# Optimization experiments

Hardware: AMD Instinct MI355X
Metric: run time of the kernel (lower is better)

Reference implementation:

```python
import jax, jax.numpy as jnp
import numpy as np

A, NA, D_OBS, B = 16, 8, 64, 128  # agents, actions, obs dim, graphs
DZ = D_OBS + NA  # obs_z_input_dim = 72


def _mlp(x, W1, b1, W2, b2):
    # Linear -> leaky_relu(0.01) -> Linear, torch Linear convention (y = x @ W.T + b)
    return jax.nn.leaky_relu(x @ W1.T + b1) @ W2.T + b2


def setup_inputs() -> dict:
    key = jax.random.key(0)
    ks = iter(jax.random.split(key, 40))
    p = {}
    p["obs"] = jax.random.normal(next(ks), (B * A, D_OBS), jnp.float32)
    p["policies"] = jax.random.uniform(next(ks), (B * A, NA), jnp.float32)
    p["actions"] = jax.random.uniform(next(ks), (B * A, NA), jnp.float32)

    def mk(name, inp, out):
        p[name + "_w"] = jax.random.normal(next(ks), (out, inp), jnp.float32) / np.sqrt(inp).astype(np.float32)
        p[name + "_b"] = jax.random.normal(next(ks), (out,), jnp.float32) * 0.01

    mk("kw1", D_OBS, 64); mk("kw2", 64, 64)   # key_weight layers
    mk("qw1", D_OBS, 64); mk("qw2", 64, 64)   # query_weight layers
    mk("ko1", DZ, 64);    mk("ko2", 64, 64)   # key_obsz layers
    mk("qo1", DZ, 64);    mk("qo2", 64, 64)   # query_obsz layers
    mk("av1", DZ, 64);    mk("av2", 64, 64)   # attention_value_obsz layers
    mk("fv1", 128, 64);   mk("fv2", 64, 8)    # final_value layers
    return p


def reference(obs, policies, actions,
              kw1_w, kw1_b, kw2_w, kw2_b, qw1_w, qw1_b, qw2_w, qw2_b,
              ko1_w, ko1_b, ko2_w, ko2_b, qo1_w, qo1_b, qo2_w, qo2_b,
              av1_w, av1_b, av2_w, av2_b, fv1_w, fv1_b, fv2_w, fv2_b):
    d_k_w = jnp.sqrt(jnp.float32(kw2_w.shape[0]))
    d_k_o = jnp.sqrt(jnp.float32(ko2_w.shape[0]))
    Bn = obs.shape[0] // A
    obs_b = obs.reshape(Bn, A, -1)                      # [B,A,Dobs]
    pi = policies.reshape(Bn, A, NA)
    act = actions.reshape(Bn, A, NA)

    # --- DGL update_all on the fully-connected (with self-loop) per-batch graph ---
    key_z = _mlp(obs_b, kw1_w, kw1_b, kw2_w, kw2_b)     # [B,A,dk]
    query_z = _mlp(obs_b, qw1_w, qw1_b, qw2_w, qw2_b)
    score = jnp.einsum('bjd,bid->bij', key_z, query_z)  # src key j -> dst query i
    w = jax.nn.sigmoid(score / d_k_w)[..., None]        # [B,A,A,1], mailbox gate
    z = w * act[:, None] + (1.0 - w) * pi[:, None]      # [B,A(i),A(j),NA]
    weight_z = w.reshape(Bn * A, A, 1)

    # obs_z[b,i,j] = cat(obs[b,j], z[b,i,j])
    obs_rep = jnp.broadcast_to(obs_b[:, None], (Bn, A, A, obs_b.shape[-1]))
    obs_z = jnp.concatenate([obs_rep, z], axis=-1)      # [B,A,A,DZ]

    diag = jnp.arange(A)
    src = obs_z[:, diag, diag]                          # source_obs_z_: [B,A,DZ] (j==i entry)

    key_o = _mlp(src, ko1_w, ko1_b, ko2_w, ko2_b)       # broadcast over j
    query_o = _mlp(obs_z, qo1_w, qo1_b, qo2_w, qo2_b)   # [B,A,A,dk]
    score_o = jnp.einsum('bid,bijd->bij', key_o, query_o)
    weights_o = jax.nn.softmax(jnp.exp(jnp.clip(score_o / d_k_o, -5.0, 5.0)), axis=-1)  # [B,A,A]

    # obs_z_pi[b,i,j,k] = op[b,j] if k==j else obs_z[b,i,k], op = cat(obs, pi)
    op = jnp.concatenate([obs_b, pi], axis=-1)          # [B,A,DZ]
    m = jnp.eye(A, dtype=obs.dtype)[None, None, :, :, None]          # (j,k) mask
    obs_z_pi = obs_z[:, :, None] * (1.0 - m) + op[:, None, None] * m  # [B,A,A,A,DZ]

    attn_src = _mlp(src, av1_w, av1_b, av2_w, av2_b)                  # [B,A,O]
    attn_other = _mlp(obs_z_pi, av1_w, av1_b, av2_w, av2_b)           # [B,A,A,A,O]

    w_exp = weights_o[:, None, :, :, None]              # [b,i,j,k,1] = weights_o[b,j,k]
    mixed = jnp.mean(attn_other * w_exp, axis=-2)       # mean over k -> [B,A,A,O]
    src_rep = jnp.broadcast_to(attn_src[:, None], mixed.shape)
    node_features = jnp.concatenate([src_rep, mixed], axis=-1)        # [B,A,A,2O]
    value = _mlp(node_features, fv1_w, fv1_b, fv2_w, fv2_b)           # [B,A,A,8]

    weights_obsz = jnp.broadcast_to(w_exp, (Bn, A, A, A, 1))
    return value, weight_z, weights_obsz
```

## Files before the change

### kernel.cpp

```cpp
#include <hip/hip_runtime.h>

#define A_ 16
#define NA_ 8
#define DOBS_ 64

typedef _Float16 f16;
typedef f16 h2 __attribute__((ext_vector_type(2)));
typedef f16 v8h __attribute__((ext_vector_type(8)));
typedef float v4f __attribute__((ext_vector_type(4)));

__device__ __forceinline__ float fdot2f(h2 a, h2 b, float c) {
  return __builtin_amdgcn_fdot2(a, b, c, false);
}
__device__ __forceinline__ float lrelu(float x) { return x > 0.f ? x : 0.01f * x; }

struct P {
  const float *obs, *pol, *act;
  const float *kw1w, *kw1b, *kw2w, *kw2b, *qw1w, *qw1b, *qw2w, *qw2b;
  const float *ko1w, *ko1b, *ko2w, *ko2b, *qo1w, *qo1b, *qo2w, *qo2b;
  const float *av1w, *av1b, *av2w, *av2b, *fv1w, *fv1b, *fv2w, *fv2b;
  float *out0, *out1, *out2;
};

struct alignas(16) SM {
  f16 obsh[16 * 72];
  float pi[128];
  float act[128];
  float wsig[256];
  float wo[256];
  float c0[16];
  f16 eh[256];
  union {
    struct {
      f16 obsl[16 * 72];
      f16 Wp1[64 * 72], Wp2[64 * 72];
      f16 Wxh[64 * 72], Wxl[64 * 72];
      f16 X1h[16 * 72], X1l[16 * 72];
      f16 X2h[16 * 72], X2l[16 * 72];
      float S2[16 * 68];
      float S3G[16 * 68];
      float wz[512];
    } f;
    struct {
      f16 AOsrcD[16 * 72];
      f16 APT[64 * 24];
      f16 AextH[16 * 40];
      f16 fv2pw[512];
      f16 slice[8][1536];
      union { struct { f16 av1H[64 * 96]; f16 av2H[64 * 72]; } av; f16 fv1H[64 * 136]; } W;
      float av1b[64], av2b[64], fv1b[64], fv2b[8];
    } bk;
  } u;
};

__device__ __forceinline__ v4f gemm_plain(const f16* Xh, const f16* W, float bv, int nt, int lane) {
  const int m = lane & 15, q = lane >> 4;
  v4f acc = {bv, bv, bv, bv};
  const v8h a0 = *(const v8h*)(Xh + m * 72 + q * 8);
  const v8h a1 = *(const v8h*)(Xh + m * 72 + 32 + q * 8);
  const f16* wr = W + (nt * 16 + m) * 72 + q * 8;
  acc = __builtin_amdgcn_mfma_f32_16x16x32_f16(a0, *(const v8h*)wr, acc, 0, 0, 0);
  acc = __builtin_amdgcn_mfma_f32_16x16x32_f16(a1, *(const v8h*)(wr + 32), acc, 0, 0, 0);
  return acc;
}

__device__ __forceinline__ v4f gemm_tile(const f16* Xh, const f16* Xl,
                                         const f16* Wh, const f16* Wl,
                                         float bv, int nt, int lane) {
  const int m = lane & 15, q = lane >> 4;
  v4f acc = {bv, bv, bv, bv};
  const v8h ah0 = *(const v8h*)(Xh + m * 72 + q * 8);
  const v8h ah1 = *(const v8h*)(Xh + m * 72 + 32 + q * 8);
  const v8h al0 = *(const v8h*)(Xl + m * 72 + q * 8);
  const v8h al1 = *(const v8h*)(Xl + m * 72 + 32 + q * 8);
  const f16* wr = Wh + (nt * 16 + m) * 72 + q * 8;
  const v8h bh0 = *(const v8h*)(wr);
  const v8h bh1 = *(const v8h*)(wr + 32);
  const f16* wr2 = Wl + (nt * 16 + m) * 72 + q * 8;
  const v8h bl0 = *(const v8h*)(wr2);
  const v8h bl1 = *(const v8h*)(wr2 + 32);
  acc = __builtin_amdgcn_mfma_f32_16x16x32_f16(ah0, bh0, acc, 0, 0, 0);
  acc = __builtin_amdgcn_mfma_f32_16x16x32_f16(ah1, bh1, acc, 0, 0, 0);
  acc = __builtin_amdgcn_mfma_f32_16x16x32_f16(ah0, bl0, acc, 0, 0, 0);
  acc = __builtin_amdgcn_mfma_f32_16x16x32_f16(ah1, bl1, acc, 0, 0, 0);
  acc = __builtin_amdgcn_mfma_f32_16x16x32_f16(al0, bh0, acc, 0, 0, 0);
  acc = __builtin_amdgcn_mfma_f32_16x16x32_f16(al1, bh1, acc, 0, 0, 0);
  return acc;
}

__device__ __forceinline__ void writeX(f16* Xh, f16* Xl, v4f acc, int nt, int lane, bool relu) {
  const int m = lane & 15, q = lane >> 4;
#pragma unroll
  for (int reg = 0; reg < 4; reg++) {
    float y = acc[reg];
    if (relu) y = lrelu(y);
    const f16 yh = (f16)y;
    Xh[(q * 4 + reg) * 72 + nt * 16 + m] = yh;
    Xl[(q * 4 + reg) * 72 + nt * 16 + m] = (f16)(y - (float)yh);
  }
}

__device__ __forceinline__ void putP(f16* W, float4 v, int o, int rq) {
  h2* d = (h2*)(W + o * 72 + 4 * rq);
  d[0] = h2{(f16)v.x, (f16)v.y};
  d[1] = h2{(f16)v.z, (f16)v.w};
}

__device__ __forceinline__ void putW(f16* Wh, f16* Wl, float4 v, int o, int rq) {
  h2* dh = (h2*)(Wh + o * 72 + 4 * rq);
  h2* dl = (h2*)(Wl + o * 72 + 4 * rq);
  const f16 hx = (f16)v.x, hy = (f16)v.y, hz = (f16)v.z, hw = (f16)v.w;
  dh[0] = h2{hx, hy};
  dh[1] = h2{hz, hw};
  dl[0] = h2{(f16)(v.x - (float)hx), (f16)(v.y - (float)hy)};
  dl[1] = h2{(f16)(v.z - (float)hz), (f16)(v.w - (float)hw)};
}

__device__ __forceinline__ v8h bfrag(const f16* Wm, int stride, int nt, int ks, int lane) {
  const int n = lane & 15, q = lane >> 4;
  return *(const v8h*)(Wm + (nt * 16 + n) * stride + ks * 32 + q * 8);
}

__device__ __forceinline__ void av_mlp2(const f16* obsh, const f16* av1H, const f16* av2H,
                                        const float* av1b, const float* av2b,
                                        f16* Hbuf, v8h az, int lane, v4f acc2[4]) {
  const int m = lane & 15, q = lane >> 4;
  const v8h a0 = *(const v8h*)(obsh + m * 72 + q * 8);
  const v8h a1 = *(const v8h*)(obsh + m * 72 + 32 + q * 8);
#pragma unroll
  for (int nt = 0; nt < 4; nt++) {
    const float bv = av1b[nt * 16 + m];
    v4f acc = {bv, bv, bv, bv};
    acc = __builtin_amdgcn_mfma_f32_16x16x32_f16(a0, bfrag(av1H, 96, nt, 0, lane), acc, 0, 0, 0);
    acc = __builtin_amdgcn_mfma_f32_16x16x32_f16(a1, bfrag(av1H, 96, nt, 1, lane), acc, 0, 0, 0);
    acc = __builtin_amdgcn_mfma_f32_16x16x32_f16(az, bfrag(av1H, 96, nt, 2, lane), acc, 0, 0, 0);
#pragma unroll
    for (int reg = 0; reg < 4; reg++)
      Hbuf[(q * 4 + reg) * 72 + nt * 16 + m] = (f16)lrelu(acc[reg]);
  }
  const v8h h0 = *(const v8h*)(Hbuf + m * 72 + q * 8);
  const v8h h1 = *(const v8h*)(Hbuf + m * 72 + 32 + q * 8);
#pragma unroll
  for (int nt = 0; nt < 4; nt++) {
    const float bv = av2b[nt * 16 + m];
    v4f acc = {bv, bv, bv, bv};
    acc = __builtin_amdgcn_mfma_f32_16x16x32_f16(h0, bfrag(av2H, 72, nt, 0, lane), acc, 0, 0, 0);
    acc = __builtin_amdgcn_mfma_f32_16x16x32_f16(h1, bfrag(av2H, 72, nt, 1, lane), acc, 0, 0, 0);
    acc2[nt] = acc;
  }
}

__global__ __launch_bounds__(512) void critic_fused(P p) {
  __shared__ SM s;
  const int tid = threadIdx.x;
  const int b = blockIdx.x >> 1, ihalf = blockIdx.x & 1;
  const int w = tid >> 6, lane = tid & 63;
  const int m = lane & 15, quad = lane >> 4;
  const int o = tid & 63, r8 = tid >> 6;

  float4 Rkw1[2], Rkw2[2], Rqw1[2], Rqw2[2], Rko2[2], Rko1[2], Rqo1[2], Rqo2[2];
#pragma unroll
  for (int h = 0; h < 2; h++) {
    const int rq = r8 + 8 * h;
    Rkw1[h] = *(const float4*)(p.kw1w + o * 64 + 4 * rq);
    Rkw2[h] = *(const float4*)(p.kw2w + o * 64 + 4 * rq);
    Rqw1[h] = *(const float4*)(p.qw1w + o * 64 + 4 * rq);
    Rqw2[h] = *(const float4*)(p.qw2w + o * 64 + 4 * rq);
    Rko2[h] = *(const float4*)(p.ko2w + o * 64 + 4 * rq);
    Rko1[h] = *(const float4*)(p.ko1w + o * 72 + 4 * rq);
    Rqo1[h] = *(const float4*)(p.qo1w + o * 72 + 4 * rq);
    Rqo2[h].x = p.qo2w[(4 * rq + 0) * 64 + o];
    Rqo2[h].y = p.qo2w[(4 * rq + 1) * 64 + o];
    Rqo2[h].z = p.qo2w[(4 * rq + 2) * 64 + o];
    Rqo2[h].w = p.qo2w[(4 * rq + 3) * 64 + o];
  }
  const float Rwzko = p.ko1w[(tid >> 3) * 72 + 64 + (tid & 7)];
  const float Rwzqo = p.qo1w[(tid >> 3) * 72 + 64 + (tid & 7)];
  const int bi = (w & 3) * 16 + m;
  const float bias1 = (w < 4 ? p.kw1b : p.qw1b)[bi];
  const float bias2 = (w < 4 ? p.kw2b : p.qw2b)[bi];
  const float bias3 = (w < 4 ? p.ko1b : p.qo1b)[bi];
  const float bias4 = p.ko2b[bi];
  const float Bqo2_0 = p.qo2b[tid & 31];
  const float Bqo2_1 = p.qo2b[(tid & 31) + 32];
  const float4 rav1a = ((const float4*)p.av1w)[tid * 2];
  const float4 rav1b = ((const float4*)p.av1w)[tid * 2 + 1];
  const float rav1c = p.av1w[4096 + tid];
  const float4 rav2a = ((const float4*)p.av2w)[tid * 2];
  const float4 rav2b = ((const float4*)p.av2w)[tid * 2 + 1];
  float4 rfv[4];
#pragma unroll
  for (int qq = 0; qq < 4; qq++) rfv[qq] = ((const float4*)p.fv1w)[tid * 4 + qq];
  const float rfv2 = p.fv2w[tid];
  float rb1 = 0.f, rb2 = 0.f, rb3 = 0.f, rb4 = 0.f;
  if (tid < 64) { rb1 = p.av1b[tid]; rb2 = p.av2b[tid]; rb3 = p.fv1b[tid]; }
  if (tid < 8) rb4 = p.fv2b[tid];

  {
    const float2 ov = ((const float2*)(p.obs + (size_t)b * 1024))[tid];
    const int e0 = 2 * tid, r0 = e0 >> 6, c0i = e0 & 63;
    const f16 hx = (f16)ov.x, hy = (f16)ov.y;
    *(h2*)(s.obsh + r0 * 72 + c0i) = h2{hx, hy};
    *(h2*)(s.u.f.obsl + r0 * 72 + c0i) = h2{(f16)(ov.x - (float)hx), (f16)(ov.y - (float)hy)};
  }
  if (tid < 128) s.pi[tid] = p.pol[(size_t)b * 128 + tid];
  else if (tid < 256) s.act[tid - 128] = p.act[(size_t)b * 128 + tid - 128];
  s.u.f.wz[tid] = Rwzko;
  putP(s.u.f.Wp1, Rkw1[0], o, r8); putP(s.u.f.Wp1, Rkw1[1], o, r8 + 8);
  putP(s.u.f.Wp2, Rqw1[0], o, r8); putP(s.u.f.Wp2, Rqw1[1], o, r8 + 8);
  putW(s.u.f.Wxh, s.u.f.Wxl, Rko1[0], o, r8); putW(s.u.f.Wxh, s.u.f.Wxl, Rko1[1], o, r8 + 8);
  __syncthreads();

  {
    const f16* Wp = (w < 4) ? s.u.f.Wp1 : s.u.f.Wp2;
    f16* Xo = (w < 4) ? s.u.f.X1h : s.u.f.X2h;
    v4f a = gemm_plain(s.obsh, Wp, bias1, w & 3, lane);
#pragma unroll
    for (int reg = 0; reg < 4; reg++)
      Xo[(quad * 4 + reg) * 72 + (w & 3) * 16 + m] = (f16)lrelu(a[reg]);
  }
  __syncthreads();
  putP(s.u.f.Wp1, Rkw2[0], o, r8); putP(s.u.f.Wp1, Rkw2[1], o, r8 + 8);
  putP(s.u.f.Wp2, Rqw2[0], o, r8); putP(s.u.f.Wp2, Rqw2[1], o, r8 + 8);
  __syncthreads();

  {
    const f16* Wp = (w < 4) ? s.u.f.Wp1 : s.u.f.Wp2;
    const f16* Xi = (w < 4) ? s.u.f.X1h : s.u.f.X2h;
    float* So = (w < 4) ? s.u.f.S2 : s.u.f.S3G;
    v4f a = gemm_plain(Xi, Wp, bias2, w & 3, lane);
#pragma unroll
    for (int reg = 0; reg < 4; reg++)
      So[(quad * 4 + reg) * 68 + (w & 3) * 16 + m] = a[reg];
  }
  __syncthreads();

  {
    const int idx = tid >> 1, g2 = tid & 1;
    const int i = idx >> 4, j = idx & 15;
    float a0 = 0.f, a1 = 0.f, a2 = 0.f, a3 = 0.f;
#pragma unroll
    for (int t4 = 0; t4 < 8; t4++) {
      const float4 qv = *(const float4*)(s.u.f.S3G + i * 68 + g2 * 32 + 4 * t4);
      const float4 kv = *(const float4*)(s.u.f.S2 + j * 68 + g2 * 32 + 4 * t4);
      a0 += qv.x * kv.x; a1 += qv.y * kv.y; a2 += qv.z * kv.z; a3 += qv.w * kv.w;
    }
    float sc = (a0 + a1) + (a2 + a3);
    sc += __shfl_xor(sc, 1);
    if (g2 == 0) {
      const float wv = 1.f / (1.f + __expf(-sc * 0.125f));
      s.wsig[idx] = wv;
      p.out1[(size_t)b * 256 + idx] = wv;
    }
    putW(s.u.f.Wp1, s.u.f.Wp2, Rqo1[0], o, r8);
    putW(s.u.f.Wp1, s.u.f.Wp2, Rqo1[1], o, r8 + 8);
  }
  __syncthreads();

  if (w < 4) {
    v4f a = gemm_tile(s.obsh, s.u.f.obsl, s.u.f.Wxh, s.u.f.Wxl, bias3, w, lane);
    const int oo = w * 16 + m;
    float wzv[8];
    *(float4*)wzv = *(const float4*)(s.u.f.wz + oo * 8);
    *(float4*)(wzv + 4) = *(const float4*)(s.u.f.wz + oo * 8 + 4);
#pragma unroll
    for (int reg = 0; reg < 4; reg++) {
      const int rr = quad * 4 + reg;
      const float wrr = s.wsig[rr * 16 + rr];
      float zp = 0.f;
#pragma unroll
      for (int c = 0; c < 8; c++) {
        const float zc = s.pi[rr * 8 + c] + wrr * (s.act[rr * 8 + c] - s.pi[rr * 8 + c]);
        zp += wzv[c] * zc;
      }
      const float y = lrelu(a[reg] + zp);
      const f16 yh = (f16)y;
      s.u.f.X2h[rr * 72 + oo] = yh;
      s.u.f.X2l[rr * 72 + oo] = (f16)(y - (float)yh);
    }
  } else {
    v4f a = gemm_tile(s.obsh, s.u.f.obsl, s.u.f.Wp1, s.u.f.Wp2, bias3, w - 4, lane);
#pragma unroll
    for (int reg = 0; reg < 4; reg++)
      s.u.f.S3G[m * 68 + (quad * 4 + reg) * 4 + (w - 4)] = a[reg];
  }
  __syncthreads();

  putW(s.u.f.Wxh, s.u.f.Wxl, Rko2[0], o, r8); putW(s.u.f.Wxh, s.u.f.Wxl, Rko2[1], o, r8 + 8);
  putW(s.u.f.Wp1, s.u.f.Wp2, Rqo2[0], o, r8); putW(s.u.f.Wp1, s.u.f.Wp2, Rqo2[1], o, r8 + 8);
  { const int oo = tid >> 3, c = tid & 7; s.u.f.wz[(oo & 15) * 32 + (oo >> 4) * 8 + c] = Rwzqo; }
  __syncthreads();

  if (w < 4) {
    v4f a = gemm_tile(s.u.f.X2h, s.u.f.X2l, s.u.f.Wxh, s.u.f.Wxl, bias4, w, lane);
    writeX(s.u.f.X1h, s.u.f.X1l, a, w, lane, false);
  }
  __syncthreads();

  if (w < 4) {
    v4f a = gemm_tile(s.u.f.X1h, s.u.f.X1l, s.u.f.Wp1, s.u.f.Wp2, 0.f, w, lane);
#pragma unroll
    for (int reg = 0; reg < 4; reg++)
      s.u.f.S2[(quad * 4 + reg) * 68 + w * 16 + m] = a[reg];
  }
  {
    const int rr = tid >> 5, cc = tid & 31;
    const float kv0 = (float)s.u.f.X1h[rr * 72 + cc] + (float)s.u.f.X1l[rr * 72 + cc];
    const float kv1 = (float)s.u.f.X1h[rr * 72 + cc + 32] + (float)s.u.f.X1l[rr * 72 + cc + 32];
    float t = kv0 * Bqo2_0 + kv1 * Bqo2_1;
#pragma unroll
    for (int mk = 1; mk < 32; mk <<= 1) t += __shfl_xor(t, mk);
    if (cc == 0) s.c0[rr] = t;
  }
  __syncthreads();

  {
    const int idx = tid >> 1, g2 = tid & 1;
    const int i = idx >> 4, j = idx & 15;
    const float wij = s.wsig[i * 16 + j];
    float z[8];
#pragma unroll
    for (int c = 0; c < 8; c++) z[c] = s.pi[j * 8 + c] + wij * (s.act[j * 8 + c] - s.pi[j * 8 + c]);
    float sc = 0.f;
#pragma unroll
    for (int gg = 2 * g2; gg <= 2 * g2 + 1; gg++) {
#pragma unroll
      for (int t = 0; t < 16; t++) {
        const float4 wa = *(const float4*)(s.u.f.wz + t * 32 + gg * 8);
        const float4 wb = *(const float4*)(s.u.f.wz + t * 32 + gg * 8 + 4);
        float hv = s.u.f.S3G[t * 68 + j * 4 + gg]
          + wa.x * z[0] + wa.y * z[1] + wa.z * z[2] + wa.w * z[3]
          + wb.x * z[4] + wb.y * z[5] + wb.z * z[6] + wb.w * z[7];
        hv = lrelu(hv);
        sc += s.u.f.S2[i * 68 + gg * 16 + t] * hv;
      }
    }
    sc += __shfl_xor(sc, 1);
    if (g2 == 0) {
      float yv = (sc + s.c0[i]) * 0.125f;
      yv = fminf(fmaxf(yv, -5.f), 5.f);
      s.eh[idx] = (f16)__expf(yv);
    }
  }
  __syncthreads();

  if (tid < 256) {
    const int i = tid >> 4, j = tid & 15;
    float ev[16]; float mx = -1e30f;
#pragma unroll
    for (int jj = 0; jj < 16; jj++) { ev[jj] = (float)s.eh[i * 16 + jj]; mx = fmaxf(mx, ev[jj]); }
    float den = 0.f;
#pragma unroll
    for (int jj = 0; jj < 16; jj++) den += __expf(ev[jj] - mx);
    s.wo[tid] = __expf(ev[j] - mx) / den;
  }
  {
    float av1v[8] = {rav1a.x, rav1a.y, rav1a.z, rav1a.w, rav1b.x, rav1b.y, rav1b.z, rav1b.w};
#pragma unroll
    for (int e = 0; e < 8; e++) {
      const int k = tid * 8 + e, rr = k / 72, cc = k - rr * 72;
      s.u.bk.W.av.av1H[rr * 96 + cc] = (f16)av1v[e];
    }
    const int k = 4096 + tid, rr = k / 72, cc = k - rr * 72;
    s.u.bk.W.av.av1H[rr * 96 + cc] = (f16)rav1c;
    const int row = tid >> 3, c0p = 72 + (tid & 7) * 3;
#pragma unroll
    for (int c = 0; c < 3; c++) s.u.bk.W.av.av1H[row * 96 + c0p + c] = (f16)0.f;
    float av2v[8] = {rav2a.x, rav2a.y, rav2a.z, rav2a.w, rav2b.x, rav2b.y, rav2b.z, rav2b.w};
#pragma unroll
    for (int e = 0; e < 8; e++) {
      const int k2 = tid * 8 + e;
      s.u.bk.W.av.av2H[(k2 >> 6) * 72 + (k2 & 63)] = (f16)av2v[e];
    }
    s.u.bk.fv2pw[tid] = (f16)rfv2;
    if (tid < 64) { s.u.bk.av1b[tid] = rb1; s.u.bk.av2b[tid] = rb2; s.u.bk.fv1b[tid] = rb3; }
    if (tid < 8) s.u.bk.fv2b[tid] = rb4;
  }
  __syncthreads();

  {
    const int kk = tid >> 5, j2 = tid & 31;
    float v = 0.f;
    if (j2 < 16) v = s.wo[kk * 16 + j2] * 0.0625f;
    else if (j2 - 16 == kk) v = s.wo[kk * 16 + kk] * 0.0625f;
    s.u.bk.AextH[kk * 40 + j2] = (f16)v;
    const int q_ = tid >> 1, g2_ = tid & 1, k_ = q_ & 15;
    float* dst = p.out2 + ((size_t)b * 256 + q_) * 16 + 8 * g2_;
    *(float4*)(dst) = *(const float4*)(s.wo + k_ * 16 + 8 * g2_);
    *(float4*)(dst + 4) = *(const float4*)(s.wo + k_ * 16 + 8 * g2_ + 4);
  }
  __syncthreads();

  const int i_ = ihalf * 8 + w;
  f16* Sl = &s.u.bk.slice[w][0];
  {
    v8h az = {};
    if (quad == 0) {
      const float wv = s.wsig[i_ * 16 + m];
#pragma unroll
      for (int c = 0; c < 8; c++)
        az[c] = (f16)(s.pi[m * 8 + c] + wv * (s.act[m * 8 + c] - s.pi[m * 8 + c]));
    }
    v4f acc2[4];
    av_mlp2(s.obsh, s.u.bk.W.av.av1H, s.u.bk.W.av.av2H, s.u.bk.av1b, s.u.bk.av2b, Sl, az, lane, acc2);
#pragma unroll
    for (int nt = 0; nt < 4; nt++)
#pragma unroll
      for (int reg = 0; reg < 4; reg++)
        Sl[(nt * 16 + m) * 24 + quad * 4 + reg] = (f16)acc2[nt][reg];
  }
  if (w == 0) {
    v8h az = {};
    if (quad == 0) {
#pragma unroll
      for (int c = 0; c < 8; c++) az[c] = (f16)s.pi[m * 8 + c];
    }
    v4f acc2[4];
    av_mlp2(s.obsh, s.u.bk.W.av.av1H, s.u.bk.W.av.av2H, s.u.bk.av1b, s.u.bk.av2b, s.u.bk.APT, az, lane, acc2);
#pragma unroll
    for (int nt = 0; nt < 4; nt++)
#pragma unroll
      for (int reg = 0; reg < 4; reg++)
        s.u.bk.APT[(nt * 16 + m) * 24 + quad * 4 + reg] = (f16)acc2[nt][reg];
  }
  if (w == 1) {
    v8h az = {};
    if (quad == 0) {
      const float wv = s.wsig[m * 16 + m];
#pragma unroll
      for (int c = 0; c < 8; c++)
        az[c] = (f16)(s.pi[m * 8 + c] + wv * (s.act[m * 8 + c] - s.pi[m * 8 + c]));
    }
    v4f acc2[4];
    av_mlp2(s.obsh, s.u.bk.W.av.av1H, s.u.bk.W.av.av2H, s.u.bk.av1b, s.u.bk.av2b, s.u.bk.AOsrcD, az, lane, acc2);
#pragma unroll
    for (int nt = 0; nt < 4; nt++)
#pragma unroll
      for (int reg = 0; reg < 4; reg++)
        s.u.bk.AOsrcD[(quad * 4 + reg) * 72 + nt * 16 + m] = (f16)acc2[nt][reg];
  }
  __syncthreads();

#pragma unroll
  for (int qq = 0; qq < 4; qq++) {
    const int e0 = tid * 16 + qq * 4;
    h2* d = (h2*)&s.u.bk.W.fv1H[(e0 >> 7) * 136 + (e0 & 127)];
    d[0] = h2{(f16)rfv[qq].x, (f16)rfv[qq].y};
    d[1] = h2{(f16)rfv[qq].z, (f16)rfv[qq].w};
  }
  __syncthreads();

  {
    const v8h am = *(const v8h*)(&s.u.bk.AextH[m * 40 + quad * 8]);
    v4f macc[4];
#pragma unroll
    for (int nt = 0; nt < 4; nt++) {
      const int oo = nt * 16 + m;
      v8h bf;
      if (quad < 2) {
        bf = *(const v8h*)(Sl + oo * 24 + quad * 8);
      } else {
        const v8h apv = *(const v8h*)(&s.u.bk.APT[oo * 24 + (quad - 2) * 8]);
        const v8h aov = *(const v8h*)(Sl + oo * 24 + (quad - 2) * 8);
        bf = apv - aov;
      }
      v4f z4 = {0.f, 0.f, 0.f, 0.f};
      macc[nt] = __builtin_amdgcn_mfma_f32_16x16x32_f16(am, bf, z4, 0, 0, 0);
    }
#pragma unroll
    for (int nt = 0; nt < 4; nt++)
#pragma unroll
      for (int reg = 0; reg < 4; reg++)
        Sl[(quad * 4 + reg) * 72 + nt * 16 + m] = (f16)macc[nt][reg];
  }
  {
    const v8h f0 = *(const v8h*)(&s.u.bk.AOsrcD[m * 72 + quad * 8]);
    const v8h f1 = *(const v8h*)(&s.u.bk.AOsrcD[m * 72 + 32 + quad * 8]);
    const v8h f2 = *(const v8h*)(Sl + m * 72 + quad * 8);
    const v8h f3 = *(const v8h*)(Sl + m * 72 + 32 + quad * 8);
#pragma unroll
    for (int nt = 0; nt < 4; nt++) {
      const float bv = s.u.bk.fv1b[nt * 16 + m];
      v4f acc = {bv, bv, bv, bv};
      acc = __builtin_amdgcn_mfma_f32_16x16x32_f16(f0, bfrag(s.u.bk.W.fv1H, 136, nt, 0, lane), acc, 0, 0, 0);
      acc = __builtin_amdgcn_mfma_f32_16x16x32_f16(f1, bfrag(s.u.bk.W.fv1H, 136, nt, 1, lane), acc, 0, 0, 0);
      acc = __builtin_amdgcn_mfma_f32_16x16x32_f16(f2, bfrag(s.u.bk.W.fv1H, 136, nt, 2, lane), acc, 0, 0, 0);
      acc = __builtin_amdgcn_mfma_f32_16x16x32_f16(f3, bfrag(s.u.bk.W.fv1H, 136, nt, 3, lane), acc, 0, 0, 0);
#pragma unroll
      for (int reg = 0; reg < 4; reg++)
        Sl[(quad * 4 + reg) * 72 + nt * 16 + m] = (f16)lrelu(acc[reg]);
    }
  }
  {
    const int g2 = quad;
    float y0 = s.u.bk.fv2b[2 * g2], y1 = s.u.bk.fv2b[2 * g2 + 1];
#pragma unroll
    for (int o2 = 0; o2 < 32; o2++) {
      const h2 hh = *(const h2*)(Sl + m * 72 + 2 * o2);
      const h2 w0 = *(const h2*)(&s.u.bk.fv2pw[(2 * g2) * 64 + 2 * o2]);
      const h2 w1 = *(const h2*)(&s.u.bk.fv2pw[(2 * g2 + 1) * 64 + 2 * o2]);
      y0 = fdot2f(w0, hh, y0);
      y1 = fdot2f(w1, hh, y1);
    }
    *(float2*)(p.out0 + ((size_t)b * 256 + i_ * 16 + m) * 8 + 2 * g2) = make_float2(y0, y1);
  }
}

extern "C" void kernel_launch(void* const* d_in, const int* in_sizes, int n_in,
                              void* d_out, int out_size, void* d_ws, size_t ws_size,
                              hipStream_t stream) {
  P p;
  p.obs = (const float*)d_in[0];
  p.pol = (const float*)d_in[1];
  p.act = (const float*)d_in[2];
  p.kw1w = (const float*)d_in[3];  p.kw1b = (const float*)d_in[4];
  p.kw2w = (const float*)d_in[5];  p.kw2b = (const float*)d_in[6];
  p.qw1w = (const float*)d_in[7];  p.qw1b = (const float*)d_in[8];
  p.qw2w = (const float*)d_in[9];  p.qw2b = (const float*)d_in[10];
  p.ko1w = (const float*)d_in[11]; p.ko1b = (const float*)d_in[12];
  p.ko2w = (const float*)d_in[13]; p.ko2b = (const float*)d_in[14];
  p.qo1w = (const float*)d_in[15]; p.qo1b = (const float*)d_in[16];
  p.qo2w = (const float*)d_in[17]; p.qo2b = (const float*)d_in[18];
  p.av1w = (const float*)d_in[19]; p.av1b = (const float*)d_in[20];
  p.av2w = (const float*)d_in[21]; p.av2b = (const float*)d_in[22];
  p.fv1w = (const float*)d_in[23]; p.fv1b = (const float*)d_in[24];
  p.fv2w = (const float*)d_in[25]; p.fv2b = (const float*)d_in[26];

  const int Bn = in_sizes[0] / (A_ * DOBS_);
  p.out0 = (float*)d_out;
  p.out1 = p.out0 + (size_t)Bn * A_ * A_ * NA_;
  p.out2 = p.out1 + (size_t)Bn * A_ * A_;

  hipLaunchKernelGGL(critic_fused, dim3(2 * Bn), dim3(512), 0, stream, p);
}
```

Measured before the change: 127.6 us.

## Stage all front-end weights into dynamic LDS upfront and drop intermediate barriers

Replaces the static shared-memory struct with a larger dynamically sized LDS buffer (about 140 KB) so every front-stage weight matrix gets its own slot. All eight weight matrices are written to LDS once at the start, which removes the staged reloads and several __syncthreads between GEMM phases. Global weight loads are also reordered and the fv1 conversion is moved earlier to trim a barrier. The larger LDS footprint keeps occupancy at one 512-thread block per CU and requires raising the dynamic shared-memory attribute.

```diff
diff --git a/kernel.cpp b/kernel.cpp
--- a/kernel.cpp
+++ b/kernel.cpp
@@ -22,36 +22,45 @@
   float *out0, *out1, *out2;
 };
 
-struct alignas(16) SM {
-  f16 obsh[16 * 72];
-  float pi[128];
-  float act[128];
-  float wsig[256];
-  float wo[256];
-  float c0[16];
-  f16 eh[256];
-  union {
-    struct {
-      f16 obsl[16 * 72];
-      f16 Wp1[64 * 72], Wp2[64 * 72];
-      f16 Wxh[64 * 72], Wxl[64 * 72];
-      f16 X1h[16 * 72], X1l[16 * 72];
-      f16 X2h[16 * 72], X2l[16 * 72];
-      float S2[16 * 68];
-      float S3G[16 * 68];
-      float wz[512];
-    } f;
-    struct {
-      f16 AOsrcD[16 * 72];
-      f16 APT[64 * 24];
-      f16 AextH[16 * 40];
-      f16 fv2pw[512];
-      f16 slice[8][1536];
-      union { struct { f16 av1H[64 * 96]; f16 av2H[64 * 72]; } av; f16 fv1H[64 * 136]; } W;
-      float av1b[64], av2b[64], fv1b[64], fv2b[8];
-    } bk;
-  } u;
-};
+#define OBSH 0
+#define OBSL 1152
+#define X1Ho 2304
+#define X1Lo 3456
+#define X2Ho 4608
+#define X2Lo 5760
+#define EHO  6912
+#define FLT  7168
+#define F_PI   0
+#define F_ACT  128
+#define F_WSIG 256
+#define F_WO   512
+#define F_C0   768
+#define F_S2   784
+#define F_S3G  1872
+#define F_WZK  2960
+#define F_WZQ  3472
+#define WKW1  15136
+#define WQW1  19744
+#define WKW2  24352
+#define WQW2  28960
+#define WKO1H 33568
+#define WKO1L 38176
+#define WKO2H 42784
+#define WKO2L 47392
+#define WQO1H 52000
+#define WQO1L 56608
+#define WQO2H 61216
+#define WQO2L 65824
+#define LDS_F16 70432
+#define AV1H  15136
+#define AV2H  21280
+#define FV1H  25888
+#define FV2PW 34592
+#define BACKB 35104
+#define SLICE 52000
+#define AOSRC 64288
+#define APTO  65440
+#define AEXT  66976
 
 __device__ __forceinline__ v4f gemm_plain(const f16* Xh, const f16* W, float bv, int nt, int lane) {
   const int m = lane & 15, q = lane >> 4;
@@ -151,31 +160,36 @@
 }
 
 __global__ __launch_bounds__(512) void critic_fused(P p) {
-  __shared__ SM s;
+  extern __shared__ f16 SMB[];
+  float* F = (float*)(SMB + FLT);
   const int tid = threadIdx.x;
   const int b = blockIdx.x >> 1, ihalf = blockIdx.x & 1;
   const int w = tid >> 6, lane = tid & 63;
   const int m = lane & 15, quad = lane >> 4;
   const int o = tid & 63, r8 = tid >> 6;
 
-  float4 Rkw1[2], Rkw2[2], Rqw1[2], Rqw2[2], Rko2[2], Rko1[2], Rqo1[2], Rqo2[2];
+  const float2 Robs = ((const float2*)(p.obs + (size_t)b * 1024))[tid];
+  float Rpa = 0.f;
+  if (tid < 128) Rpa = p.pol[(size_t)b * 128 + tid];
+  else if (tid < 256) Rpa = p.act[(size_t)b * 128 + tid - 128];
+  const float Rwzko = p.ko1w[(tid >> 3) * 72 + 64 + (tid & 7)];
+  const float Rwzqo = p.qo1w[(tid >> 3) * 72 + 64 + (tid & 7)];
+  float4 Rkw1[2], Rqw1[2], Rkw2[2], Rqw2[2], Rko1[2], Rko2[2], Rqo1[2], Rqo2[2];
 #pragma unroll
   for (int h = 0; h < 2; h++) {
     const int rq = r8 + 8 * h;
     Rkw1[h] = *(const float4*)(p.kw1w + o * 64 + 4 * rq);
+    Rqw1[h] = *(const float4*)(p.qw1w + o * 64 + 4 * rq);
     Rkw2[h] = *(const float4*)(p.kw2w + o * 64 + 4 * rq);
-    Rqw1[h] = *(const float4*)(p.qw1w + o * 64 + 4 * rq);
     Rqw2[h] = *(const float4*)(p.qw2w + o * 64 + 4 * rq);
+    Rko1[h] = *(const float4*)(p.ko1w + o * 72 + 4 * rq);
     Rko2[h] = *(const float4*)(p.ko2w + o * 64 + 4 * rq);
-    Rko1[h] = *(const float4*)(p.ko1w + o * 72 + 4 * rq);
     Rqo1[h] = *(const float4*)(p.qo1w + o * 72 + 4 * rq);
     Rqo2[h].x = p.qo2w[(4 * rq + 0) * 64 + o];
     Rqo2[h].y = p.qo2w[(4 * rq + 1) * 64 + o];
     Rqo2[h].z = p.qo2w[(4 * rq + 2) * 64 + o];
     Rqo2[h].w = p.qo2w[(4 * rq + 3) * 64 + o];
   }
-  const float Rwzko = p.ko1w[(tid >> 3) * 72 + 64 + (tid & 7)];
-  const float Rwzqo = p.qo1w[(tid >> 3) * 72 + 64 + (tid & 7)];
   const int bi = (w & 3) * 16 + m;
   const float bias1 = (w < 4 ? p.kw1b : p.qw1b)[bi];
   const float bias2 = (w < 4 ? p.kw2b : p.qw2b)[bi];
@@ -183,163 +197,163 @@
   const float bias4 = p.ko2b[bi];
   const float Bqo2_0 = p.qo2b[tid & 31];
   const float Bqo2_1 = p.qo2b[(tid & 31) + 32];
+
+  {
+    const int e0 = 2 * tid, r0 = e0 >> 6, c0i = e0 & 63;
+    const f16 hx = (f16)Robs.x, hy = (f16)Robs.y;
+    *(h2*)(SMB + OBSH + r0 * 72 + c0i) = h2{hx, hy};
+    *(h2*)(SMB + OBSL + r0 * 72 + c0i) = h2{(f16)(Robs.x - (float)hx), (f16)(Robs.y - (float)hy)};
+  }
+  if (tid < 128) F[F_PI + tid] = Rpa;
+  else if (tid < 256) F[F_ACT + tid - 128] = Rpa;
+  F[F_WZK + tid] = Rwzko;
+  { const int oo = tid >> 3, c = tid & 7; F[F_WZQ + (oo & 15) * 32 + (oo >> 4) * 8 + c] = Rwzqo; }
+#pragma unroll
+  for (int h = 0; h < 2; h++) {
+    const int rq = r8 + 8 * h;
+    putP(SMB + WKW1, Rkw1[h], o, rq);
+    putP(SMB + WQW1, Rqw1[h], o, rq);
+    putP(SMB + WKW2, Rkw2[h], o, rq);
+    putP(SMB + WQW2, Rqw2[h], o, rq);
+    putW(SMB + WKO1H, SMB + WKO1L, Rko1[h], o, rq);
+    putW(SMB + WKO2H, SMB + WKO2L, Rko2[h], o, rq);
+    putW(SMB + WQO1H, SMB + WQO1L, Rqo1[h], o, rq);
+    putW(SMB + WQO2H, SMB + WQO2L, Rqo2[h], o, rq);
+  }
+  __syncthreads();
+
+  {
+    const f16* Wp = (w < 4) ? (SMB + WKW1) : (SMB + WQW1);
+    f16* Xo = (w < 4) ? (SMB + X1Ho) : (SMB + X2Ho);
+    v4f a = gemm_plain(SMB + OBSH, Wp, bias1, w & 3, lane);
+#pragma unroll
+    for (int reg = 0; reg < 4; reg++)
+      Xo[(quad * 4 + reg) * 72 + (w & 3) * 16 + m] = (f16)lrelu(a[reg]);
+  }
+  __syncthreads();
+
+  {
+    const f16* Wp = (w < 4) ? (SMB + WKW2) : (SMB + WQW2);
+    const f16* Xi = (w < 4) ? (SMB + X1Ho) : (SMB + X2Ho);
+    float* So = (w < 4) ? (F + F_S2) : (F + F_S3G);
+    v4f a = gemm_plain(Xi, Wp, bias2, w & 3, lane);
+#pragma unroll
+    for (int reg = 0; reg < 4; reg++)
+      So[(quad * 4 + reg) * 68 + (w & 3) * 16 + m] = a[reg];
+  }
+  __syncthreads();
+
+  {
+    const int idx = tid >> 1, g2 = tid & 1;
+    const int i = idx >> 4, j = idx & 15;
+    float a0 = 0.f, a1 = 0.f, a2 = 0.f, a3 = 0.f;
+#pragma unroll
+    for (int t4 = 0; t4 < 8; t4++) {
+      const float4 qv = *(const float4*)(F + F_S3G + i * 68 + g2 * 32 + 4 * t4);
+      const float4 kv = *(const float4*)(F + F_S2 + j * 68 + g2 * 32 + 4 * t4);
+      a0 += qv.x * kv.x; a1 += qv.y * kv.y; a2 += qv.z * kv.z; a3 += qv.w * kv.w;
+    }
+    float sc = (a0 + a1) + (a2 + a3);
+    sc += __shfl_xor(sc, 1);
+    if (g2 == 0) {
+      const float wv = 1.f / (1.f + __expf(-sc * 0.125f));
+      F[F_WSIG + idx] = wv;
+      p.out1[(size_t)b * 256 + idx] = wv;
+    }
+  }
+  __syncthreads();
+
+  if (w < 4) {
+    v4f a = gemm_tile(SMB + OBSH, SMB + OBSL, SMB + WKO1H, SMB + WKO1L, bias3, w, lane);
+    const int oo = w * 16 + m;
+    float wzv[8];
+    *(float4*)wzv = *(const float4*)(F + F_WZK + oo * 8);
+    *(float4*)(wzv + 4) = *(const float4*)(F + F_WZK + oo * 8 + 4);
+#pragma unroll
+    for (int reg = 0; reg < 4; reg++) {
+      const int rr = quad * 4 + reg;
+      const float wrr = F[F_WSIG + rr * 16 + rr];
+      float zp = 0.f;
+#pragma unroll
+      for (int c = 0; c < 8; c++) {
+        const float zc = F[F_PI + rr * 8 + c] + wrr * (F[F_ACT + rr * 8 + c] - F[F_PI + rr * 8 + c]);
+        zp += wzv[c] * zc;
+      }
+      const float y = lrelu(a[reg] + zp);
+      const f16 yh = (f16)y;
+      SMB[X2Ho + rr * 72 + oo] = yh;
+      SMB[X2Lo + rr * 72 + oo] = (f16)(y - (float)yh);
+    }
+  } else {
+    v4f a = gemm_tile(SMB + OBSH, SMB + OBSL, SMB + WQO1H, SMB + WQO1L, bias3, w - 4, lane);
+#pragma unroll
+    for (int reg = 0; reg < 4; reg++)
+      F[F_S3G + m * 68 + (quad * 4 + reg) * 4 + (w - 4)] = a[reg];
+  }
+  __syncthreads();
+
   const float4 rav1a = ((const float4*)p.av1w)[tid * 2];
   const float4 rav1b = ((const float4*)p.av1w)[tid * 2 + 1];
   const float rav1c = p.av1w[4096 + tid];
   const float4 rav2a = ((const float4*)p.av2w)[tid * 2];
   const float4 rav2b = ((const float4*)p.av2w)[tid * 2 + 1];
-  float4 rfv[4];
-#pragma unroll
-  for (int qq = 0; qq < 4; qq++) rfv[qq] = ((const float4*)p.fv1w)[tid * 4 + qq];
   const float rfv2 = p.fv2w[tid];
   float rb1 = 0.f, rb2 = 0.f, rb3 = 0.f, rb4 = 0.f;
   if (tid < 64) { rb1 = p.av1b[tid]; rb2 = p.av2b[tid]; rb3 = p.fv1b[tid]; }
   if (tid < 8) rb4 = p.fv2b[tid];
-
-  {
-    const float2 ov = ((const float2*)(p.obs + (size_t)b * 1024))[tid];
-    const int e0 = 2 * tid, r0 = e0 >> 6, c0i = e0 & 63;
-    const f16 hx = (f16)ov.x, hy = (f16)ov.y;
-    *(h2*)(s.obsh + r0 * 72 + c0i) = h2{hx, hy};
-    *(h2*)(s.u.f.obsl + r0 * 72 + c0i) = h2{(f16)(ov.x - (float)hx), (f16)(ov.y - (float)hy)};
-  }
-  if (tid < 128) s.pi[tid] = p.pol[(size_t)b * 128 + tid];
-  else if (tid < 256) s.act[tid - 128] = p.act[(size_t)b * 128 + tid - 128];
-  s.u.f.wz[tid] = Rwzko;
-  putP(s.u.f.Wp1, Rkw1[0], o, r8); putP(s.u.f.Wp1, Rkw1[1], o, r8 + 8);
-  putP(s.u.f.Wp2, Rqw1[0], o, r8); putP(s.u.f.Wp2, Rqw1[1], o, r8 + 8);
-  putW(s.u.f.Wxh, s.u.f.Wxl, Rko1[0], o, r8); putW(s.u.f.Wxh, s.u.f.Wxl, Rko1[1], o, r8 + 8);
-  __syncthreads();
-
-  {
-    const f16* Wp = (w < 4) ? s.u.f.Wp1 : s.u.f.Wp2;
-    f16* Xo = (w < 4) ? s.u.f.X1h : s.u.f.X2h;
-    v4f a = gemm_plain(s.obsh, Wp, bias1, w & 3, lane);
+  if (w < 4) {
+    v4f a = gemm_tile(SMB + X2Ho, SMB + X2Lo, SMB + WKO2H, SMB + WKO2L, bias4, w, lane);
+    writeX(SMB + X1Ho, SMB + X1Lo, a, w, lane, false);
+  }
+  __syncthreads();
+
+  float4 rfv[4];
+#pragma unroll
+  for (int qq = 0; qq < 4; qq++) rfv[qq] = ((const float4*)p.fv1w)[tid * 4 + qq];
+  if (w < 4) {
+    v4f a = gemm_tile(SMB + X1Ho, SMB + X1Lo, SMB + WQO2H, SMB + WQO2L, 0.f, w, lane);
 #pragma unroll
     for (int reg = 0; reg < 4; reg++)
-      Xo[(quad * 4 + reg) * 72 + (w & 3) * 16 + m] = (f16)lrelu(a[reg]);
-  }
-  __syncthreads();
-  putP(s.u.f.Wp1, Rkw2[0], o, r8); putP(s.u.f.Wp1, Rkw2[1], o, r8 + 8);
-  putP(s.u.f.Wp2, Rqw2[0], o, r8); putP(s.u.f.Wp2, Rqw2[1], o, r8 + 8);
-  __syncthreads();
-
-  {
-    const f16* Wp = (w < 4) ? s.u.f.Wp1 : s.u.f.Wp2;
-    const f16* Xi = (w < 4) ? s.u.f.X1h : s.u.f.X2h;
-    float* So = (w < 4) ? s.u.f.S2 : s.u.f.S3G;
-    v4f a = gemm_plain(Xi, Wp, bias2, w & 3, lane);
-#pragma unroll
-    for (int reg = 0; reg < 4; reg++)
-      So[(quad * 4 + reg) * 68 + (w & 3) * 16 + m] = a[reg];
+      F[F_S2 + (quad * 4 + reg) * 68 + w * 16 + m] = a[reg];
+  }
+  {
+    const int rr = tid >> 5, cc = tid & 31;
+    const float kv0 = (float)SMB[X1Ho + rr * 72 + cc] + (float)SMB[X1Lo + rr * 72 + cc];
+    const float kv1 = (float)SMB[X1Ho + rr * 72 + cc + 32] + (float)SMB[X1Lo + rr * 72 + cc + 32];
+    float t = kv0 * Bqo2_0 + kv1 * Bqo2_1;
+#pragma unroll
+    for (int mk = 1; mk < 32; mk <<= 1) t += __shfl_xor(t, mk);
+    if (cc == 0) F[F_C0 + rr] = t;
   }
   __syncthreads();
 
   {
     const int idx = tid >> 1, g2 = tid & 1;
     const int i = idx >> 4, j = idx & 15;
-    float a0 = 0.f, a1 = 0.f, a2 = 0.f, a3 = 0.f;
-#pragma unroll
-    for (int t4 = 0; t4 < 8; t4++) {
-      const float4 qv = *(const float4*)(s.u.f.S3G + i * 68 + g2 * 32 + 4 * t4);
-      const float4 kv = *(const float4*)(s.u.f.S2 + j * 68 + g2 * 32 + 4 * t4);
-      a0 += qv.x * kv.x; a1 += qv.y * kv.y; a2 += qv.z * kv.z; a3 += qv.w * kv.w;
-    }
-    float sc = (a0 + a1) + (a2 + a3);
-    sc += __shfl_xor(sc, 1);
-    if (g2 == 0) {
-      const float wv = 1.f / (1.f + __expf(-sc * 0.125f));
-      s.wsig[idx] = wv;
-      p.out1[(size_t)b * 256 + idx] = wv;
-    }
-    putW(s.u.f.Wp1, s.u.f.Wp2, Rqo1[0], o, r8);
-    putW(s.u.f.Wp1, s.u.f.Wp2, Rqo1[1], o, r8 + 8);
-  }
-  __syncthreads();
-
-  if (w < 4) {
-    v4f a = gemm_tile(s.obsh, s.u.f.obsl, s.u.f.Wxh, s.u.f.Wxl, bias3, w, lane);
-    const int oo = w * 16 + m;
-    float wzv[8];
-    *(float4*)wzv = *(const float4*)(s.u.f.wz + oo * 8);
-    *(float4*)(wzv + 4) = *(const float4*)(s.u.f.wz + oo * 8 + 4);
-#pragma unroll
-    for (int reg = 0; reg < 4; reg++) {
-      const int rr = quad * 4 + reg;
-      const float wrr = s.wsig[rr * 16 + rr];
-      float zp = 0.f;
-#pragma unroll
-      for (int c = 0; c < 8; c++) {
-        const float zc = s.pi[rr * 8 + c] + wrr * (s.act[rr * 8 + c] - s.pi[rr * 8 + c]);
-        zp += wzv[c] * zc;
-      }
-      const float y = lrelu(a[reg] + zp);
-      const f16 yh = (f16)y;
-      s.u.f.X2h[rr * 72 + oo] = yh;
-      s.u.f.X2l[rr * 72 + oo] = (f16)(y - (float)yh);
-    }
-  } else {
-    v4f a = gemm_tile(s.obsh, s.u.f.obsl, s.u.f.Wp1, s.u.f.Wp2, bias3, w - 4, lane);
-#pragma unroll
-    for (int reg = 0; reg < 4; reg++)
-      s.u.f.S3G[m * 68 + (quad * 4 + reg) * 4 + (w - 4)] = a[reg];
-  }
-  __syncthreads();
-
-  putW(s.u.f.Wxh, s.u.f.Wxl, Rko2[0], o, r8); putW(s.u.f.Wxh, s.u.f.Wxl, Rko2[1], o, r8 + 8);
-  putW(s.u.f.Wp1, s.u.f.Wp2, Rqo2[0], o, r8); putW(s.u.f.Wp1, s.u.f.Wp2, Rqo2[1], o, r8 + 8);
-  { const int oo = tid >> 3, c = tid & 7; s.u.f.wz[(oo & 15) * 32 + (oo >> 4) * 8 + c] = Rwzqo; }
-  __syncthreads();
-
-  if (w < 4) {
-    v4f a = gemm_tile(s.u.f.X2h, s.u.f.X2l, s.u.f.Wxh, s.u.f.Wxl, bias4, w, lane);
-    writeX(s.u.f.X1h, s.u.f.X1l, a, w, lane, false);
-  }
-  __syncthreads();
-
-  if (w < 4) {
-    v4f a = gemm_tile(s.u.f.X1h, s.u.f.X1l, s.u.f.Wp1, s.u.f.Wp2, 0.f, w, lane);
-#pragma unroll
-    for (int reg = 0; reg < 4; reg++)
-      s.u.f.S2[(quad * 4 + reg) * 68 + w * 16 + m] = a[reg];
-  }
-  {
-    const int rr = tid >> 5, cc = tid & 31;
-    const float kv0 = (float)s.u.f.X1h[rr * 72 + cc] + (float)s.u.f.X1l[rr * 72 + cc];
-    const float kv1 = (float)s.u.f.X1h[rr * 72 + cc + 32] + (float)s.u.f.X1l[rr * 72 + cc + 32];
-    float t = kv0 * Bqo2_0 + kv1 * Bqo2_1;
-#pragma unroll
-    for (int mk = 1; mk < 32; mk <<= 1) t += __shfl_xor(t, mk);
-    if (cc == 0) s.c0[rr] = t;
-  }
-  __syncthreads();
-
-  {
-    const int idx = tid >> 1, g2 = tid & 1;
-    const int i = idx >> 4, j = idx & 15;
-    const float wij = s.wsig[i * 16 + j];
+    const float wij = F[F_WSIG + i * 16 + j];
     float z[8];
 #pragma unroll
-    for (int c = 0; c < 8; c++) z[c] = s.pi[j * 8 + c] + wij * (s.act[j * 8 + c] - s.pi[j * 8 + c]);
+    for (int c = 0; c < 8; c++)
+      z[c] = F[F_PI + j * 8 + c] + wij * (F[F_ACT + j * 8 + c] - F[F_PI + j * 8 + c]);
     float sc = 0.f;
 #pragma unroll
     for (int gg = 2 * g2; gg <= 2 * g2 + 1; gg++) {
 #pragma unroll
       for (int t = 0; t < 16; t++) {
-        const float4 wa = *(const float4*)(s.u.f.wz + t * 32 + gg * 8);
-        const float4 wb = *(const float4*)(s.u.f.wz + t * 32 + gg * 8 + 4);
-        float hv = s.u.f.S3G[t * 68 + j * 4 + gg]
+        const float4 wa = *(const float4*)(F + F_WZQ + t * 32 + gg * 8);
+        const float4 wb = *(const float4*)(F + F_WZQ + t * 32 + gg * 8 + 4);
+        float hv = F[F_S3G + t * 68 + j * 4 + gg]
           + wa.x * z[0] + wa.y * z[1] + wa.z * z[2] + wa.w * z[3]
           + wb.x * z[4] + wb.y * z[5] + wb.z * z[6] + wb.w * z[7];
         hv = lrelu(hv);
-        sc += s.u.f.S2[i * 68 + gg * 16 + t] * hv;
+        sc += F[F_S2 + i * 68 + gg * 16 + t] * hv;
       }
     }
     sc += __shfl_xor(sc, 1);
     if (g2 == 0) {
-      float yv = (sc + s.c0[i]) * 0.125f;
+      float yv = (sc + F[F_C0 + i]) * 0.125f;
       yv = fminf(fmaxf(yv, -5.f), 5.f);
-      s.eh[idx] = (f16)__expf(yv);
+      SMB[EHO + idx] = (f16)__expf(yv);
     }
   }
   __syncthreads();
@@ -348,61 +362,70 @@
     const int i = tid >> 4, j = tid & 15;
     float ev[16]; float mx = -1e30f;
 #pragma unroll
-    for (int jj = 0; jj < 16; jj++) { ev[jj] = (float)s.eh[i * 16 + jj]; mx = fmaxf(mx, ev[jj]); }
+    for (int jj = 0; jj < 16; jj++) { ev[jj] = (float)SMB[EHO + i * 16 + jj]; mx = fmaxf(mx, ev[jj]); }
     float den = 0.f;
 #pragma unroll
     for (int jj = 0; jj < 16; jj++) den += __expf(ev[jj] - mx);
-    s.wo[tid] = __expf(ev[j] - mx) / den;
+    F[F_WO + tid] = __expf(ev[j] - mx) / den;
   }
   {
     float av1v[8] = {rav1a.x, rav1a.y, rav1a.z, rav1a.w, rav1b.x, rav1b.y, rav1b.z, rav1b.w};
 #pragma unroll
     for (int e = 0; e < 8; e++) {
       const int k = tid * 8 + e, rr = k / 72, cc = k - rr * 72;
-      s.u.bk.W.av.av1H[rr * 96 + cc] = (f16)av1v[e];
+      SMB[AV1H + rr * 96 + cc] = (f16)av1v[e];
     }
     const int k = 4096 + tid, rr = k / 72, cc = k - rr * 72;
-    s.u.bk.W.av.av1H[rr * 96 + cc] = (f16)rav1c;
+    SMB[AV1H + rr * 96 + cc] = (f16)rav1c;
     const int row = tid >> 3, c0p = 72 + (tid & 7) * 3;
 #pragma unroll
-    for (int c = 0; c < 3; c++) s.u.bk.W.av.av1H[row * 96 + c0p + c] = (f16)0.f;
+    for (int c = 0; c < 3; c++) SMB[AV1H + row * 96 + c0p + c] = (f16)0.f;
     float av2v[8] = {rav2a.x, rav2a.y, rav2a.z, rav2a.w, rav2b.x, rav2b.y, rav2b.z, rav2b.w};
 #pragma unroll
     for (int e = 0; e < 8; e++) {
       const int k2 = tid * 8 + e;
-      s.u.bk.W.av.av2H[(k2 >> 6) * 72 + (k2 & 63)] = (f16)av2v[e];
-    }
-    s.u.bk.fv2pw[tid] = (f16)rfv2;
-    if (tid < 64) { s.u.bk.av1b[tid] = rb1; s.u.bk.av2b[tid] = rb2; s.u.bk.fv1b[tid] = rb3; }
-    if (tid < 8) s.u.bk.fv2b[tid] = rb4;
+      SMB[AV2H + (k2 >> 6) * 72 + (k2 & 63)] = (f16)av2v[e];
+    }
+    SMB[FV2PW + tid] = (f16)rfv2;
+    float* BF = (float*)(SMB + BACKB);
+    if (tid < 64) { BF[tid] = rb1; BF[64 + tid] = rb2; BF[128 + tid] = rb3; }
+    if (tid < 8) BF[192 + tid] = rb4;
   }
   __syncthreads();
 
   {
     const int kk = tid >> 5, j2 = tid & 31;
     float v = 0.f;
-    if (j2 < 16) v = s.wo[kk * 16 + j2] * 0.0625f;
-    else if (j2 - 16 == kk) v = s.wo[kk * 16 + kk] * 0.0625f;
-    s.u.bk.AextH[kk * 40 + j2] = (f16)v;
+    if (j2 < 16) v = F[F_WO + kk * 16 + j2] * 0.0625f;
+    else if (j2 - 16 == kk) v = F[F_WO + kk * 16 + kk] * 0.0625f;
+    SMB[AEXT + kk * 40 + j2] = (f16)v;
     const int q_ = tid >> 1, g2_ = tid & 1, k_ = q_ & 15;
     float* dst = p.out2 + ((size_t)b * 256 + q_) * 16 + 8 * g2_;
-    *(float4*)(dst) = *(const float4*)(s.wo + k_ * 16 + 8 * g2_);
-    *(float4*)(dst + 4) = *(const float4*)(s.wo + k_ * 16 + 8 * g2_ + 4);
-  }
-  __syncthreads();
-
+    *(float4*)(dst) = *(const float4*)(F + F_WO + k_ * 16 + 8 * g2_);
+    *(float4*)(dst + 4) = *(const float4*)(F + F_WO + k_ * 16 + 8 * g2_ + 4);
+  }
+  __syncthreads();
+
+#pragma unroll
+  for (int qq = 0; qq < 4; qq++) {
+    const int e0 = tid * 16 + qq * 4;
+    h2* d = (h2*)&SMB[FV1H + (e0 >> 7) * 136 + (e0 & 127)];
+    d[0] = h2{(f16)rfv[qq].x, (f16)rfv[qq].y};
+    d[1] = h2{(f16)rfv[qq].z, (f16)rfv[qq].w};
+  }
+  const float* BF = (const float*)(SMB + BACKB);
   const int i_ = ihalf * 8 + w;
-  f16* Sl = &s.u.bk.slice[w][0];
+  f16* Sl = SMB + SLICE + w * 1536;
   {
     v8h az = {};
     if (quad == 0) {
-      const float wv = s.wsig[i_ * 16 + m];
+      const float wv = F[F_WSIG + i_ * 16 + m];
 #pragma unroll
       for (int c = 0; c < 8; c++)
-        az[c] = (f16)(s.pi[m * 8 + c] + wv * (s.act[m * 8 + c] - s.pi[m * 8 + c]));
+        az[c] = (f16)(F[F_PI + m * 8 + c] + wv * (F[F_ACT + m * 8 + c] - F[F_PI + m * 8 + c]));
     }
     v4f acc2[4];
-    av_mlp2(s.obsh, s.u.bk.W.av.av1H, s.u.bk.W.av.av2H, s.u.bk.av1b, s.u.bk.av2b, Sl, az, lane, acc2);
+    av_mlp2(SMB + OBSH, SMB + AV1H, SMB + AV2H, BF, BF + 64, Sl, az, lane, acc2);
 #pragma unroll
     for (int nt = 0; nt < 4; nt++)
 #pragma unroll
@@ -413,45 +436,36 @@
     v8h az = {};
     if (quad == 0) {
 #pragma unroll
-      for (int c = 0; c < 8; c++) az[c] = (f16)s.pi[m * 8 + c];
+      for (int c = 0; c < 8; c++) az[c] = (f16)F[F_PI + m * 8 + c];
     }
     v4f acc2[4];
-    av_mlp2(s.obsh, s.u.bk.W.av.av1H, s.u.bk.W.av.av2H, s.u.bk.av1b, s.u.bk.av2b, s.u.bk.APT, az, lane, acc2);
+    av_mlp2(SMB + OBSH, SMB + AV1H, SMB + AV2H, BF, BF + 64, SMB + APTO, az, lane, acc2);
 #pragma unroll
     for (int nt = 0; nt < 4; nt++)
 #pragma unroll
       for (int reg = 0; reg < 4; reg++)
-        s.u.bk.APT[(nt * 16 + m) * 24 + quad * 4 + reg] = (f16)acc2[nt][reg];
+        SMB[APTO + (nt * 16 + m) * 24 + quad * 4 + reg] = (f16)acc2[nt][reg];
   }
   if (w == 1) {
     v8h az = {};
     if (quad == 0) {
-      const float wv = s.wsig[m * 16 + m];
+      const float wv = F[F_WSIG + m * 16 + m];
 #pragma unroll
       for (int c = 0; c < 8; c++)
-        az[c] = (f16)(s.pi[m * 8 + c] + wv * (s.act[m * 8 + c] - s.pi[m * 8 + c]));
+        az[c] = (f16)(F[F_PI + m * 8 + c] + wv * (F[F_ACT + m * 8 + c] - F[F_PI + m * 8 + c]));
     }
     v4f acc2[4];
-    av_mlp2(s.obsh, s.u.bk.W.av.av1H, s.u.bk.W.av.av2H, s.u.bk.av1b, s.u.bk.av2b, s.u.bk.AOsrcD, az, lane, acc2);
+    av_mlp2(SMB + OBSH, SMB + AV1H, SMB + AV2H, BF, BF + 64, SMB + AOSRC, az, lane, acc2);
 #pragma unroll
     for (int nt = 0; nt < 4; nt++)
 #pragma unroll
       for (int reg = 0; reg < 4; reg++)
-        s.u.bk.AOsrcD[(quad * 4 + reg) * 72 + nt * 16 + m] = (f16)acc2[nt][reg];
-  }
-  __syncthreads();
-
-#pragma unroll
-  for (int qq = 0; qq < 4; qq++) {
-    const int e0 = tid * 16 + qq * 4;
-    h2* d = (h2*)&s.u.bk.W.fv1H[(e0 >> 7) * 136 + (e0 & 127)];
-    d[0] = h2{(f16)rfv[qq].x, (f16)rfv[qq].y};
-    d[1] = h2{(f16)rfv[qq].z, (f16)rfv[qq].w};
-  }
-  __syncthreads();
-
-  {
-    const v8h am = *(const v8h*)(&s.u.bk.AextH[m * 40 + quad * 8]);
+        SMB[AOSRC + (quad * 4 + reg) * 72 + nt * 16 + m] = (f16)acc2[nt][reg];
+  }
+  __syncthreads();
+
+  {
+    const v8h am = *(const v8h*)(&SMB[AEXT + m * 40 + quad * 8]);
     v4f macc[4];
 #pragma unroll
     for (int nt = 0; nt < 4; nt++) {
@@ -460,7 +474,7 @@
       if (quad < 2) {
         bf = *(const v8h*)(Sl + oo * 24 + quad * 8);
       } else {
-        const v8h apv = *(const v8h*)(&s.u.bk.APT[oo * 24 + (quad - 2) * 8]);
+        const v8h apv = *(const v8h*)(&SMB[APTO + oo * 24 + (quad - 2) * 8]);
         const v8h aov = *(const v8h*)(Sl + oo * 24 + (quad - 2) * 8);
         bf = apv - aov;
       }
@@ -474,18 +488,18 @@
         Sl[(quad * 4 + reg) * 72 + nt * 16 + m] = (f16)macc[nt][reg];
   }
   {
-    const v8h f0 = *(const v8h*)(&s.u.bk.AOsrcD[m * 72 + quad * 8]);
-    const v8h f1 = *(const v8h*)(&s.u.bk.AOsrcD[m * 72 + 32 + quad * 8]);
+    const v8h f0 = *(const v8h*)(&SMB[AOSRC + m * 72 + quad * 8]);
+    const v8h f1 = *(const v8h*)(&SMB[AOSRC + m * 72 + 32 + quad * 8]);
     const v8h f2 = *(const v8h*)(Sl + m * 72 + quad * 8);
     const v8h f3 = *(const v8h*)(Sl + m * 72 + 32 + quad * 8);
 #pragma unroll
     for (int nt = 0; nt < 4; nt++) {
-      const float bv = s.u.bk.fv1b[nt * 16 + m];
+      const float bv = BF[128 + nt * 16 + m];
       v4f acc = {bv, bv, bv, bv};
-      acc = __builtin_amdgcn_mfma_f32_16x16x32_f16(f0, bfrag(s.u.bk.W.fv1H, 136, nt, 0, lane), acc, 0, 0, 0);
-      acc = __builtin_amdgcn_mfma_f32_16x16x32_f16(f1, bfrag(s.u.bk.W.fv1H, 136, nt, 1, lane), acc, 0, 0, 0);
-      acc = __builtin_amdgcn_mfma_f32_16x16x32_f16(f2, bfrag(s.u.bk.W.fv1H, 136, nt, 2, lane), acc, 0, 0, 0);
-      acc = __builtin_amdgcn_mfma_f32_16x16x32_f16(f3, bfrag(s.u.bk.W.fv1H, 136, nt, 3, lane), acc, 0, 0, 0);
+      acc = __builtin_amdgcn_mfma_f32_16x16x32_f16(f0, bfrag(SMB + FV1H, 136, nt, 0, lane), acc, 0, 0, 0);
+      acc = __builtin_amdgcn_mfma_f32_16x16x32_f16(f1, bfrag(SMB + FV1H, 136, nt, 1, lane), acc, 0, 0, 0);
+      acc = __builtin_amdgcn_mfma_f32_16x16x32_f16(f2, bfrag(SMB + FV1H, 136, nt, 2, lane), acc, 0, 0, 0);
+      acc = __builtin_amdgcn_mfma_f32_16x16x32_f16(f3, bfrag(SMB + FV1H, 136, nt, 3, lane), acc, 0, 0, 0);
 #pragma unroll
       for (int reg = 0; reg < 4; reg++)
         Sl[(quad * 4 + reg) * 72 + nt * 16 + m] = (f16)lrelu(acc[reg]);
@@ -493,12 +507,12 @@
   }
   {
     const int g2 = quad;
-    float y0 = s.u.bk.fv2b[2 * g2], y1 = s.u.bk.fv2b[2 * g2 + 1];
+    float y0 = BF[192 + 2 * g2], y1 = BF[192 + 2 * g2 + 1];
 #pragma unroll
     for (int o2 = 0; o2 < 32; o2++) {
       const h2 hh = *(const h2*)(Sl + m * 72 + 2 * o2);
-      const h2 w0 = *(const h2*)(&s.u.bk.fv2pw[(2 * g2) * 64 + 2 * o2]);
-      const h2 w1 = *(const h2*)(&s.u.bk.fv2pw[(2 * g2 + 1) * 64 + 2 * o2]);
+      const h2 w0 = *(const h2*)(&SMB[FV2PW + (2 * g2) * 64 + 2 * o2]);
+      const h2 w1 = *(const h2*)(&SMB[FV2PW + (2 * g2 + 1) * 64 + 2 * o2]);
       y0 = fdot2f(w0, hh, y0);
       y1 = fdot2f(w1, hh, y1);
     }
@@ -531,5 +545,8 @@
   p.out1 = p.out0 + (size_t)Bn * A_ * A_ * NA_;
   p.out2 = p.out1 + (size_t)Bn * A_ * A_;
 
-  hipLaunchKernelGGL(critic_fused, dim3(2 * Bn), dim3(512), 0, stream, p);
-}
+  const size_t lds_bytes = (size_t)LDS_F16 * sizeof(f16);
+  (void)hipFuncSetAttribute(reinterpret_cast<const void*>(critic_fused),
+                            hipFuncAttributeMaxDynamicSharedMemorySize, (int)lds_bytes);
+  hipLaunchKernelGGL(critic_fused, dim3(2 * Bn), dim3(512), lds_bytes, stream, p);
+}
```

New measurement: 125.3 us. Within noise of the previous version (-1.8%).
